# Kernel optimization log

Measured on AMD Instinct MI355X. Metric: run time of the kernel, lower is better.

## Reference

```python
import jax, jax.numpy as jnp
import numpy as np

B, S, IN, D, H, L, DFF, NT, K = 32, 512, 256, 512, 8, 2, 2048, 424, 25
DK = D // H


def moving_avg_trend(x, k):
    # AvgPool1d(kernel=k, stride=1, pad=k//2, count_include_pad=False) along seq axis
    b, s, d = x.shape
    half = k // 2
    cs = jnp.cumsum(x, axis=1)
    cs = jnp.concatenate([jnp.zeros((b, 1, d), x.dtype), cs], axis=1)  # [b, s+1, d]
    idx = jnp.arange(s)
    hi = jnp.minimum(idx + half + 1, s)
    lo = jnp.maximum(idx - half, 0)
    win = cs[:, hi] - cs[:, lo]                    # windowed sums [b, s, d]
    cnt = (hi - lo).astype(x.dtype)
    return win / cnt[None, :, None]


def auto_correlation(x, qkvo_w, qkvo_b):
    b, s, d = x.shape
    Q = (x @ qkvo_w[0] + qkvo_b[0]).reshape(b, s, H, DK)
    Kt = (x @ qkvo_w[1] + qkvo_b[1]).reshape(b, s, H, DK)
    V = (x @ qkvo_w[2] + qkvo_b[2]).reshape(b, s, H, DK)
    Qf = jnp.fft.rfft(Q, axis=1)
    Kf = jnp.fft.rfft(Kt, axis=1)
    corr = jnp.fft.irfft(Qf * jnp.conj(Kf), n=s, axis=1)
    corr = jax.nn.softmax(corr, axis=1)
    out = (corr * V).reshape(b, s, d)
    return out @ qkvo_w[3] + qkvo_b[3]


def encoder_layer(x, qkvo_w, qkvo_b, w1, b1, w2, b2):
    x_corr = auto_correlation(x, qkvo_w, qkvo_b)
    y = x + x_corr
    x = y - moving_avg_trend(y, K)                 # seasonal component (decomp1)
    ffn = jax.nn.gelu(x @ w1 + b1) @ w2 + b2
    y = x + ffn
    x = y - moving_avg_trend(y, K)                 # decomp2
    return x


def setup_inputs() -> dict:
    key = jax.random.key(0)
    ks = jax.random.split(key, 16)
    sc = 0.02
    return {
        "x": jax.random.normal(ks[0], (B, S, IN), jnp.float32),
        "embed_w": jax.random.normal(ks[1], (IN, D), jnp.float32) * sc,
        "embed_b": jnp.zeros((D,), jnp.float32),
        "qkvo_w": jax.random.normal(ks[2], (L, 4, D, D), jnp.float32) * sc,
        "qkvo_b": jnp.zeros((L, 4, D), jnp.float32),
        "ffn_w1": jax.random.normal(ks[3], (L, D, DFF), jnp.float32) * sc,
        "ffn_b1": jnp.zeros((L, DFF), jnp.float32),
        "ffn_w2": jax.random.normal(ks[4], (L, DFF, D), jnp.float32) * sc,
        "ffn_b2": jnp.zeros((L, D), jnp.float32),
        "proj_w1": jax.random.normal(ks[5], (D, D // 2), jnp.float32) * sc,
        "proj_b1": jnp.zeros((D // 2,), jnp.float32),
        "proj_w2": jax.random.normal(ks[6], (D // 2, NT), jnp.float32) * sc,
        "proj_b2": jnp.zeros((NT,), jnp.float32),
    }


def reference(x, embed_w, embed_b, qkvo_w, qkvo_b, ffn_w1, ffn_b1, ffn_w2, ffn_b2,
              proj_w1, proj_b1, proj_w2, proj_b2):
    h = x @ embed_w + embed_b
    for l in range(L):
        h = encoder_layer(h, qkvo_w[l], qkvo_b[l], ffn_w1[l], ffn_b1[l], ffn_w2[l], ffn_b2[l])
    h = h.mean(axis=1)                             # [B, D]
    h = jax.nn.relu(h @ proj_w1 + proj_b1)
    return h @ proj_w2 + proj_b2                   # [B, NT]
```

## Files before the change

### kernel.cpp

```cpp
#include <hip/hip_runtime.h>
#include <hip/hip_bf16.h>

#define S_LEN 512
#define D_DIM 512
#define B_DIM 32
#define IN_DIM 256
#define DFF_DIM 2048
#define NT_DIM 424

static constexpr size_t SZ = (size_t)B_DIM * S_LEN * D_DIM;

using s8v = __attribute__((ext_vector_type(8))) short;
using f4v = __attribute__((ext_vector_type(4))) float;
typedef unsigned short ushortT;

__device__ __forceinline__ ushortT f2bf(float f) {
  unsigned u = __float_as_uint(f);
  u += 0x7FFFu + ((u >> 16) & 1u);
  return (ushortT)(u >> 16);
}
__device__ __forceinline__ float bf2f(ushortT h) {
  return __uint_as_float(((unsigned)h) << 16);
}

__device__ __forceinline__ float gelu_fast(float x) {
  float a = 1.5957691216057308f * (x + 0.044715f * x * x * x);
  return x / (1.f + __expf(-a));
}

__device__ __forceinline__ float2 cadd(float2 a, float2 b) { return float2{a.x + b.x, a.y + b.y}; }
__device__ __forceinline__ float2 csub(float2 a, float2 b) { return float2{a.x - b.x, a.y - b.y}; }
__device__ __forceinline__ float2 cmul(float2 a, float2 b) {
  return float2{a.x * b.x - a.y * b.y, a.x * b.y + a.y * b.x};
}
__device__ __forceinline__ float2 mni(float2 a) { return float2{a.y, -a.x}; }

__device__ __forceinline__ void dft8(float2 a[8]) {
  float2 t0 = cadd(a[0], a[4]), t4 = csub(a[0], a[4]);
  float2 t1 = cadd(a[1], a[5]), t5 = csub(a[1], a[5]);
  float2 t2 = cadd(a[2], a[6]), t6 = csub(a[2], a[6]);
  float2 t3 = cadd(a[3], a[7]), t7 = csub(a[3], a[7]);
  float2 u0 = cadd(t0, t2), u2 = csub(t0, t2);
  float2 u1 = cadd(t1, t3), u3 = csub(t1, t3);
  const float C = 0.70710678118654752f;
  float2 s5 = float2{C * (t5.x + t5.y), C * (t5.y - t5.x)};
  float2 s6 = mni(t6);
  float2 s7 = float2{C * (t7.y - t7.x), -C * (t7.x + t7.y)};
  float2 v0 = cadd(t4, s6), v2 = csub(t4, s6);
  float2 v1 = cadd(s5, s7), v3 = csub(s5, s7);
  a[0] = cadd(u0, u1); a[4] = csub(u0, u1);
  a[2] = cadd(u2, mni(u3)); a[6] = csub(u2, mni(u3));
  a[1] = cadd(v0, v1); a[5] = csub(v0, v1);
  a[3] = cadd(v2, mni(v3)); a[7] = csub(v2, mni(v3));
}

__global__ __launch_bounds__(256) void conv_all(
    const float* __restrict__ embed_w, const float* __restrict__ qkvo_w,
    const float* __restrict__ ffn_w1, const float* __restrict__ ffn_w2,
    ushortT* __restrict__ embed_wt, ushortT* __restrict__ qkvo_wt,
    ushortT* __restrict__ ffn1_wt, ushortT* __restrict__ ffn2_wt)
{
  __shared__ float T[32][33];
  const int z = blockIdx.z;
  const float* W; ushortT* Wt; int Kp, N;
  if (z == 0)       { W = embed_w; Wt = embed_wt; Kp = 256; N = 512; }
  else if (z <= 8)  { int i = z - 1; W = qkvo_w + (size_t)i * 512 * 512;
                      Wt = qkvo_wt + (size_t)i * 512 * 512; Kp = 512; N = 512; }
  else if (z <= 10) { int l = z - 9; W = ffn_w1 + (size_t)l * 512 * 2048;
                      Wt = ffn1_wt + (size_t)l * 2048 * 512; Kp = 512; N = 2048; }
  else              { int l = z - 11; W = ffn_w2 + (size_t)l * 2048 * 512;
                      Wt = ffn2_wt + (size_t)l * 512 * 2048; Kp = 2048; N = 512; }
  int k0, n0;
  if (z >= 11) { k0 = blockIdx.y * 32; n0 = blockIdx.x * 32; }
  else         { k0 = blockIdx.x * 32; n0 = blockIdx.y * 32; }
  if (k0 >= Kp || n0 >= N) return;

  const int tid = threadIdx.x;
  const int col = tid & 31, r8 = tid >> 5;
#pragma unroll
  for (int it = 0; it < 4; ++it) {
    int row = r8 + it * 8;
    T[row][col] = W[(size_t)(k0 + row) * N + n0 + col];
  }
  __syncthreads();
  const int nl = tid >> 3, kq = tid & 7;
#pragma unroll
  for (int j = 0; j < 4; ++j) {
    int kl = kq * 4 + j;
    Wt[(size_t)(n0 + nl) * Kp + k0 + kl] = f2bf(T[kl][nl]);
  }
}

__global__ __launch_bounds__(256) void cvt_bf16(
    const float* __restrict__ in, ushortT* __restrict__ out, int n4)
{
  int i = blockIdx.x * 256 + threadIdx.x;
  if (i >= n4) return;
  float4 v = ((const float4*)in)[i];
  ushortT o[4] = {f2bf(v.x), f2bf(v.y), f2bf(v.z), f2bf(v.w)};
  *(uint2*)&out[(size_t)i * 4] = *(const uint2*)o;
}

template<int ACT, int RES, int OUT>
__global__ __launch_bounds__(256) void gemm_bf16(
    const ushortT* __restrict__ A, const ushortT* __restrict__ Wt,
    const float* __restrict__ bias, const float* __restrict__ res,
    const ushortT* __restrict__ resb,
    float* __restrict__ C, ushortT* __restrict__ Cb,
    ushortT* __restrict__ Qh, ushortT* __restrict__ Kh, int M, int Kp, int N)
{
  __shared__ __align__(16) ushortT smem[24576];
  ushortT* Tt = smem;

  const int tid = threadIdx.x;
  const int lane = tid & 63, wid = tid >> 6;
  const int fr = lane & 15, kq = lane >> 4;
  const int wr = wid >> 1, wc = wid & 1;

  const int nwg = gridDim.x * gridDim.y;
  const int bid = blockIdx.y * gridDim.x + blockIdx.x;
  const int swz = (bid & 7) * (nwg >> 3) + (bid >> 3);
  const int bx = swz % gridDim.x, by = swz / gridDim.x;
  const int m0 = by * 128, n0 = bx * 128;

  int srow[2], skq[2];
#pragma unroll
  for (int t = 0; t < 2; ++t) {
    int ch = wid * 2 + t;
    int row = ch * 16 + (lane >> 2);
    int kql = lane & 3;
    srow[t] = row;
    skq[t] = kql ^ ((row >> 1) & 3);
  }

  int aoff[4], boff[4];
#pragma unroll
  for (int i = 0; i < 4; ++i) {
    int ra = wr * 64 + i * 16 + fr;
    aoff[i] = ra * 32 + ((kq ^ ((ra >> 1) & 3)) << 3);
    int rb = wc * 64 + i * 16 + fr;
    boff[i] = rb * 32 + ((kq ^ ((rb >> 1) & 3)) << 3);
  }

  auto STAGE = [&](int buf, int k0) {
#pragma unroll
    for (int t = 0; t < 2; ++t) {
      const ushortT* as = A + (size_t)(m0 + srow[t]) * Kp + k0 + skq[t] * 8;
      __builtin_amdgcn_global_load_lds(
          (const __attribute__((address_space(1))) unsigned int*)as,
          (__attribute__((address_space(3))) unsigned int*)&smem[buf * 4096 + (wid * 2 + t) * 512],
          16, 0, 0);
      const ushortT* wsrc = Wt + (size_t)(n0 + srow[t]) * Kp + k0 + skq[t] * 8;
      __builtin_amdgcn_global_load_lds(
          (const __attribute__((address_space(1))) unsigned int*)wsrc,
          (__attribute__((address_space(3))) unsigned int*)&smem[12288 + buf * 4096 + (wid * 2 + t) * 512],
          16, 0, 0);
    }
  };

  f4v acc[4][4] = {};
  STAGE(0, 0);
  if (Kp > 32) STAGE(1, 32);
  int cur = 0, nxt = 2;

  for (int k0 = 0; k0 < Kp; k0 += 32) {
    if (k0 + 32 < Kp) {
      asm volatile("s_waitcnt vmcnt(4)" ::: "memory");
    } else {
      asm volatile("s_waitcnt vmcnt(0)" ::: "memory");
    }
    __builtin_amdgcn_s_barrier();
    __builtin_amdgcn_sched_barrier(0);
    if (k0 + 64 < Kp) {
      STAGE(nxt, k0 + 64);
      nxt = (nxt == 2) ? 0 : nxt + 1;
    }
    s8v af[4], bfv[4];
    const int ab = cur * 4096, wb = 12288 + cur * 4096;
#pragma unroll
    for (int i = 0; i < 4; ++i) {
      af[i]  = *(const s8v*)&smem[ab + aoff[i]];
      bfv[i] = *(const s8v*)&smem[wb + boff[i]];
    }
#pragma unroll
    for (int i = 0; i < 4; ++i)
#pragma unroll
      for (int j = 0; j < 4; ++j)
        acc[i][j] = __builtin_amdgcn_mfma_f32_16x16x32_bf16(af[i], bfv[j], acc[i][j], 0, 0, 0);
    cur = (cur == 2) ? 0 : cur + 1;
  }

  if (OUT == 3 && n0 < 1024) {
    __syncthreads();
#pragma unroll
    for (int j = 0; j < 4; ++j) {
      const int c = wc * 64 + j * 16 + fr;
      const float bv = bias[n0 + c];
#pragma unroll
      for (int i = 0; i < 4; ++i)
#pragma unroll
        for (int r = 0; r < 4; ++r) {
          const int s = wr * 64 + i * 16 + kq * 4 + r;
          _Float16 hh = (_Float16)(acc[i][j][r] + bv);
          Tt[c * 132 + s] = __builtin_bit_cast(ushortT, hh);
        }
    }
    __syncthreads();
    ushortT* dstM = (n0 < 512) ? Qh : Kh;
    const int cg0 = n0 & 511;
    const int bb = m0 >> 9, ss0 = m0 & 511;
    const int g = tid >> 4, ln = tid & 15;
#pragma unroll
    for (int p = 0; p < 8; ++p) {
      const int c = p * 16 + g;
      uint4 v = *(const uint4*)&Tt[c * 132 + ln * 8];
      *(uint4*)&dstM[((size_t)bb * 512 + cg0 + c) * 512 + ss0 + ln * 8] = v;
    }
  } else {
    constexpr bool WB16 = (OUT != 0);
    const int nb  = (OUT == 3) ? 512 : N;
    const int cb0 = (OUT == 3) ? (n0 - 1024) : n0;
    if (WB16) __syncthreads();
#pragma unroll
    for (int j = 0; j < 4; ++j) {
      const int lc = wc * 64 + j * 16 + fr;
      const int gc = n0 + lc;
      const float bv = bias[gc];
#pragma unroll
      for (int i = 0; i < 4; ++i)
#pragma unroll
        for (int r = 0; r < 4; ++r) {
          const int lr = wr * 64 + i * 16 + kq * 4 + r;
          const int gr = m0 + lr;
          float v = acc[i][j][r] + bv;
          if (RES == 1) v += res[(size_t)gr * N + gc];
          if (RES == 2) v += bf2f(resb[(size_t)gr * N + gc]);
          if (ACT == 1) v = gelu_fast(v);
          if (OUT == 0 || OUT == 1) C[(size_t)gr * N + gc] = v;
          if (WB16) Tt[lr * 132 + lc] = f2bf(v);
        }
    }
    if (WB16) {
      __syncthreads();
      const int g = tid >> 4, ln = tid & 15;
#pragma unroll
      for (int p = 0; p < 8; ++p) {
        const int row = p * 16 + g;
        uint4 v = *(const uint4*)&Tt[row * 132 + ln * 8];
        *(uint4*)&Cb[(size_t)(m0 + row) * nb + cb0 + ln * 8] = v;
      }
    }
  }
}

__global__ __launch_bounds__(512) void autocorr_fft(
    const ushortT* __restrict__ Qh, const ushortT* __restrict__ Kh,
    const ushortT* __restrict__ Vb, ushortT* __restrict__ Ob)
{
  __shared__ float2 zs[8 * 578];
  const int tid = threadIdx.x;
  const int b  = blockIdx.x >> 6;
  const int c0 = (blockIdx.x & 63) << 3;
  const int ch = tid >> 6;
  const int t  = tid & 63;
  float2* zc = &zs[ch * 578];

  {
    const ushortT* Qg = Qh + ((size_t)b * 512 + c0 + ch) * 512 + t * 8;
    const ushortT* Kg = Kh + ((size_t)b * 512 + c0 + ch) * 512 + t * 8;
    uint4 qv = *(const uint4*)Qg;
    uint4 kv = *(const uint4*)Kg;
    const ushortT* qp = (const ushortT*)&qv;
    const ushortT* kp = (const ushortT*)&kv;
    const int base = 9 * t;
#pragma unroll
    for (int j = 0; j < 8; ++j) {
      zc[base + j] = float2{(float)__builtin_bit_cast(_Float16, qp[j]),
                            (float)__builtin_bit_cast(_Float16, kp[j])};
    }
  }
  __syncthreads();

  float2 a[8];
  auto stage_fn = [&](int stage, bool do_scatter) {
#pragma unroll
    for (int r = 0; r < 8; ++r) { int ci = t + 64 * r; a[r] = zc[ci + (ci >> 3)]; }
    dft8(a);
    if (stage < 2) {
      float angle = (stage == 0) ? (-6.283185307179586f / 512.f) * (float)t
                                 : (-6.283185307179586f / 64.f) * (float)(t >> 3);
      float sn, cs;
      __sincosf(angle, &sn, &cs);
      float2 w = float2{cs, sn}, wp = w;
      a[1] = cmul(a[1], wp);
#pragma unroll
      for (int r = 2; r < 8; ++r) { wp = cmul(wp, w); a[r] = cmul(a[r], wp); }
    }
    if (!do_scatter) return;
    __syncthreads();
#pragma unroll
    for (int r = 0; r < 8; ++r) {
      int ci = (stage == 0) ? 8 * t + r
             : (stage == 1) ? (t & 7) + 64 * (t >> 3) + 8 * r
                            : t + 64 * r;
      zc[ci + (ci >> 3)] = a[r];
    }
    __syncthreads();
  };

  stage_fn(0, true); stage_fn(1, true); stage_fn(2, true);

  float2 Zk[8], Zm[8];
#pragma unroll
  for (int r = 0; r < 8; ++r) {
    int k = t + 64 * r, mk = (512 - k) & 511;
    Zk[r] = zc[k + (k >> 3)];
    Zm[r] = zc[mk + (mk >> 3)];
  }
  __syncthreads();
  const float S = 0.00048828125f;
#pragma unroll
  for (int r = 0; r < 8; ++r) {
    int k = t + 64 * r;
    float x1 = Zk[r].x, y1 = Zk[r].y, x2 = Zm[r].x, y2 = Zm[r].y;
    float sx = x1 + x2, dx = x1 - x2, sy = y1 + y2, dy = y1 - y2;
    float pre = sx * sy - dy * dx;
    float pim = sx * dx + dy * sy;
    zc[k + (k >> 3)] = float2{pre * S, -pim * S};
  }
  __syncthreads();

  stage_fn(0, true); stage_fn(1, true); stage_fn(2, false);

  float corr[8];
#pragma unroll
  for (int r = 0; r < 8; ++r) corr[r] = a[r].x;
  float mx = corr[0];
#pragma unroll
  for (int r = 1; r < 8; ++r) mx = fmaxf(mx, corr[r]);
#pragma unroll
  for (int o = 1; o < 64; o <<= 1) mx = fmaxf(mx, __shfl_xor(mx, o));
  float ex[8], sum = 0.f;
#pragma unroll
  for (int r = 0; r < 8; ++r) { ex[r] = __expf(corr[r] - mx); sum += ex[r]; }
#pragma unroll
  for (int o = 1; o < 64; o <<= 1) sum += __shfl_xor(sum, o);
  const float inv = 1.f / sum;

  __syncthreads();
  float* wl = (float*)zc;
#pragma unroll
  for (int r = 0; r < 8; ++r) wl[t + 64 * r] = ex[r] * inv;
  __syncthreads();

  const float* wall = (const float*)zs;
  const size_t base = (size_t)b * S_LEN * D_DIM + c0;
  for (int i = tid; i < 4096; i += 512) {
    int s = i >> 3, cc = i & 7;
    float wv = wall[cc * 1156 + s];
    size_t ad = base + (size_t)s * D_DIM + cc;
    Ob[ad] = f2bf(wv * bf2f(Vb[ad]));
  }
}

template<int MEAN, int WF>
__global__ __launch_bounds__(256) void movavg_sub2(
    const float* __restrict__ y, float* __restrict__ outf,
    ushortT* __restrict__ outb, float* __restrict__ hm)
{
  __shared__ float ys[512 * 32];
  const int tid = threadIdx.x;
  const int b = blockIdx.y, d0 = blockIdx.x * 32;
  const float* yb = y + (size_t)b * S_LEN * D_DIM + d0;

#pragma unroll 4
  for (int p = 0; p < 16; ++p) {
    int i = p * 256 + tid;
    int s = i >> 3, dq = i & 7;
    float4 v = *(const float4*)(yb + (size_t)s * D_DIM + dq * 4);
    *(float4*)&ys[s * 32 + dq * 4] = v;
  }
  __syncthreads();

  const int d = tid & 31, sg = tid >> 5;
  const int s0 = sg * 64;
  int lo = max(s0 - 12, 0), hi = min(s0 + 13, S_LEN);
  float sum = 0.f;
  for (int t = lo; t < hi; ++t) sum += ys[t * 32 + d];

  float msum = 0.f;
  const size_t gb = (size_t)b * S_LEN * D_DIM + d0 + d;
  for (int i = 0; i < 64; ++i) {
    const int s = s0 + i;
    float val = ys[s * 32 + d] - sum / (float)(hi - lo);
    size_t g = gb + (size_t)s * D_DIM;
    if (WF) outf[g] = val;
    outb[g] = f2bf(val);
    if (MEAN) msum += val;
    int add = s + 13;
    if (add < S_LEN) { sum += ys[add * 32 + d]; hi = add + 1; }
    int rem = s - 12;
    if (rem >= 0) { sum -= ys[rem * 32 + d]; lo = rem + 1; }
  }
  if (MEAN) atomicAdd(&hm[b * D_DIM + d0 + d], msum * (1.f / (float)S_LEN));
}

__global__ __launch_bounds__(256) void proj_head1(
    const float* __restrict__ hm, const float* __restrict__ W1,
    const float* __restrict__ b1, float* __restrict__ p1)
{
  __shared__ float hs[32 * 512];
  const int tid = threadIdx.x, n0 = blockIdx.x * 32;
  for (int i = tid; i < 16384; i += 256) hs[i] = hm[i];
  __syncthreads();
  const int n = tid & 31, mg = tid >> 5;
  float acc[4] = {};
  for (int k = 0; k < 512; ++k) {
    float w = W1[(size_t)k * 256 + n0 + n];
#pragma unroll
    for (int mi = 0; mi < 4; ++mi)
      acc[mi] = fmaf(hs[(mg * 4 + mi) * 512 + k], w, acc[mi]);
  }
  const float bb = b1[n0 + n];
#pragma unroll
  for (int mi = 0; mi < 4; ++mi)
    p1[(size_t)(mg * 4 + mi) * 256 + n0 + n] = fmaxf(acc[mi] + bb, 0.f);
}

__global__ __launch_bounds__(256) void proj_head2(
    const float* __restrict__ p1, const float* __restrict__ W2,
    const float* __restrict__ b2, float* __restrict__ out)
{
  __shared__ float ps[32 * 256];
  const int tid = threadIdx.x;
  for (int i = tid; i < 8192; i += 256) ps[i] = p1[i];
  __syncthreads();
  const int n = tid & 31, mg = tid >> 5;
  const int ng = blockIdx.x * 32 + n;
  const bool ok = ng < NT_DIM;
  float acc[4] = {};
  for (int k = 0; k < 256; ++k) {
    float w = ok ? W2[(size_t)k * NT_DIM + ng] : 0.f;
#pragma unroll
    for (int mi = 0; mi < 4; ++mi)
      acc[mi] = fmaf(ps[(mg * 4 + mi) * 256 + k], w, acc[mi]);
  }
  if (ok) {
    const float bb = b2[ng];
#pragma unroll
    for (int mi = 0; mi < 4; ++mi)
      out[(size_t)(mg * 4 + mi) * NT_DIM + ng] = acc[mi] + bb;
  }
}

extern "C" void kernel_launch(void* const* d_in, const int* in_sizes, int n_in,
                              void* d_out, int out_size, void* d_ws, size_t ws_size,
                              hipStream_t stream)
{
  const float* x       = (const float*)d_in[0];
  const float* embed_w = (const float*)d_in[1];
  const float* embed_b = (const float*)d_in[2];
  const float* qkvo_w  = (const float*)d_in[3];
  const float* qkvo_b  = (const float*)d_in[4];
  const float* ffn_w1  = (const float*)d_in[5];
  const float* ffn_b1  = (const float*)d_in[6];
  const float* ffn_w2  = (const float*)d_in[7];
  const float* ffn_b2  = (const float*)d_in[8];
  const float* proj_w1 = (const float*)d_in[9];
  const float* proj_b1 = (const float*)d_in[10];
  const float* proj_w2 = (const float*)d_in[11];
  const float* proj_b2 = (const float*)d_in[12];
  float* out = (float*)d_out;

  float* ws = (float*)d_ws;
  float* Bv = ws;
  float* Bh = ws + SZ;
  float* Bq = ws + 2 * SZ;
  float* Bk = ws + 3 * SZ;
  ushortT* Sb = (ushortT*)(ws + 4 * SZ);
  ushortT* Wb = (ushortT*)(ws + 4 * SZ + SZ / 2);
  ushortT* embed_wt = Wb;
  ushortT* qkvo_wt  = embed_wt + (size_t)512 * 256;
  ushortT* ffn1_wt  = qkvo_wt + (size_t)8 * 512 * 512;
  ushortT* ffn2_wt  = ffn1_wt + (size_t)2 * 2048 * 512;
  float* hm = (float*)(ffn2_wt + (size_t)2 * 512 * 2048);
  float* p1 = hm + 16384;
  ushortT* Hb  = (ushortT*)Bv;
  ushortT* Vb  = (ushortT*)Bv;
  ushortT* xb  = (ushortT*)Bq;
  ushortT* QKh = (ushortT*)Bq;

  dim3 blk(256);

  hipMemsetAsync(hm, 0, 16384 * sizeof(float), stream);

  conv_all<<<dim3(16, 64, 13), blk, 0, stream>>>(
      embed_w, qkvo_w, ffn_w1, ffn_w2, embed_wt, qkvo_wt, ffn1_wt, ffn2_wt);

  cvt_bf16<<<dim3(4096), blk, 0, stream>>>(x, xb, B_DIM * S_LEN * IN_DIM / 4);

  gemm_bf16<0, 0, 1><<<dim3(4, 128), blk, 0, stream>>>(
      xb, embed_wt, embed_b, nullptr, nullptr, Bh, Sb, nullptr, nullptr,
      16384, IN_DIM, D_DIM);

  for (int l = 0; l < 2; ++l) {
    const ushortT* qw = qkvo_wt + (size_t)l * 4 * 512 * 512;
    const float* qb = qkvo_b + (size_t)l * 4 * 512;
    gemm_bf16<0, 0, 3><<<dim3(12, 128), blk, 0, stream>>>(
        Sb, qw, qb, nullptr, nullptr, nullptr, Vb, QKh, QKh + SZ,
        16384, 512, 1536);
    autocorr_fft<<<dim3(B_DIM * 64), dim3(512), 0, stream>>>(QKh, QKh + SZ, Vb, Sb);
    gemm_bf16<0, 1, 0><<<dim3(4, 128), blk, 0, stream>>>(
        Sb, qw + (size_t)3 * 512 * 512, qb + 1536, Bh, nullptr, Bq, nullptr,
        nullptr, nullptr, 16384, 512, 512);
    movavg_sub2<0, 0><<<dim3(16, 32), blk, 0, stream>>>(Bq, nullptr, Sb, nullptr);
    gemm_bf16<1, 0, 2><<<dim3(16, 128), blk, 0, stream>>>(
        Sb, ffn1_wt + (size_t)l * 2048 * 512, ffn_b1 + (size_t)l * DFF_DIM,
        nullptr, nullptr, nullptr, Hb, nullptr, nullptr, 16384, 512, 2048);
    gemm_bf16<0, 2, 0><<<dim3(4, 128), blk, 0, stream>>>(
        Hb, ffn2_wt + (size_t)l * 512 * 2048, ffn_b2 + (size_t)l * D_DIM,
        nullptr, Sb, Bq, nullptr, nullptr, nullptr, 16384, 2048, 512);
    if (l == 1)
      movavg_sub2<1, 1><<<dim3(16, 32), blk, 0, stream>>>(Bq, Bh, Sb, hm);
    else
      movavg_sub2<0, 1><<<dim3(16, 32), blk, 0, stream>>>(Bq, Bh, Sb, nullptr);
  }

  proj_head1<<<dim3(8), blk, 0, stream>>>(hm, proj_w1, proj_b1, p1);
  proj_head2<<<dim3(14), blk, 0, stream>>>(p1, proj_w2, proj_b2, out);
}
```

Before: 553.3 us.

## Add 256x256-tile pipelined FFN1 GEMM with direct global-to-LDS loads

Replaces the generic 128-tile bf16 GEMM for the first FFN projection with a dedicated kernel. It uses 256x256 output tiles, 512 threads, double-buffered LDS filled through global_load_lds, and four phases per K step with explicit vmcnt waits and barriers. It also adds an XOR-swizzled LDS layout, a block-id swizzle for L2 locality, and a fused bias+GELU epilogue staged through LDS. The aim is more operand reuse per tile and overlap of loads with MFMA work. The cost is 128 KB of dynamic LDS and heavy register use, which limits occupancy and relies on hand-tuned wait counts.

```diff
diff --git a/kernel.cpp b/kernel.cpp
--- a/kernel.cpp
+++ b/kernel.cpp
@@ -253,6 +253,142 @@
   }
 }
 
+__global__ __launch_bounds__(512, 2) void gemm_ffn1_256(
+    const ushortT* __restrict__ A, const ushortT* __restrict__ Wt,
+    const float* __restrict__ bias, ushortT* __restrict__ Cb,
+    int M, int Kp, int N)
+{
+  extern __shared__ ushortT smem[];
+  const int tid = threadIdx.x;
+  const int lane = tid & 63, wid = tid >> 6;
+  const int fr = lane & 15, kq = lane >> 4;
+  const int wm = wid >> 2, wn = wid & 3;
+
+  const int nwg = gridDim.x * gridDim.y;
+  const int bid = blockIdx.y * gridDim.x + blockIdx.x;
+  const int swz = (bid & 7) * (nwg >> 3) + (bid >> 3);
+  const int bx = swz % gridDim.x, by = swz / gridDim.x;
+  const int m0 = by * 256, n0 = bx * 256;
+
+  const int KT = Kp >> 6;
+
+  const int srow = wid * 8 + (lane >> 3);
+  const int sch = (lane & 7) ^ ((lane >> 3) & 7);
+
+  auto STAGE_A = [&](int b, int u, int kt) {
+    const ushortT* src = A + (size_t)(m0 + u * 64 + srow) * Kp + kt * 64 + sch * 8;
+    __builtin_amdgcn_global_load_lds(
+        (const __attribute__((address_space(1))) unsigned int*)src,
+        (__attribute__((address_space(3))) unsigned int*)
+            &smem[((b * 2 + (u >> 1)) * 128 + (u & 1) * 64) * 64 + wid * 512],
+        16, 0, 0);
+  };
+  auto STAGE_B = [&](int b, int u, int kt) {
+    const ushortT* src = Wt + (size_t)(n0 + u * 64 + srow) * Kp + kt * 64 + sch * 8;
+    __builtin_amdgcn_global_load_lds(
+        (const __attribute__((address_space(1))) unsigned int*)src,
+        (__attribute__((address_space(3))) unsigned int*)
+            &smem[32768 + ((b * 2 + (u >> 1)) * 128 + (u & 1) * 64) * 64 + wid * 512],
+        16, 0, 0);
+  };
+
+  f4v acc[8][4] = {};
+  s8v bcar[2][2];
+
+  STAGE_A(0, 0, 0); STAGE_A(0, 2, 0);
+  STAGE_B(0, 0, 0); STAGE_B(0, 1, 0);
+  STAGE_A(0, 1, 0); STAGE_A(0, 3, 0);
+  STAGE_B(0, 2, 0); STAGE_B(0, 3, 0);
+
+  auto phase = [&](int ph, int b, bool st, int kt) {
+    if (st) {
+      if (ph == 0)      { STAGE_A(b ^ 1, 0, kt + 1); STAGE_A(b ^ 1, 2, kt + 1); }
+      else if (ph == 1) { STAGE_B(b ^ 1, 0, kt + 1); STAGE_B(b ^ 1, 1, kt + 1); }
+      else if (ph == 2) { STAGE_A(b ^ 1, 1, kt + 1); STAGE_A(b ^ 1, 3, kt + 1); }
+      else              { STAGE_B(b ^ 1, 2, kt + 1); STAGE_B(b ^ 1, 3, kt + 1); }
+    }
+    if (st) {
+      asm volatile("s_waitcnt vmcnt(6)" ::: "memory");
+    } else {
+      if (ph == 0)      asm volatile("s_waitcnt vmcnt(4)" ::: "memory");
+      else if (ph == 1) asm volatile("s_waitcnt vmcnt(2)" ::: "memory");
+      else if (ph == 2) asm volatile("s_waitcnt vmcnt(0)" ::: "memory");
+    }
+    __builtin_amdgcn_s_barrier();
+    asm volatile("" ::: "memory");
+
+    const int i0 = (ph & 1) * 4;
+    const int jp = ph >> 1;
+    if ((ph & 1) == 0) {
+#pragma unroll
+      for (int jj = 0; jj < 2; ++jj) {
+        int col = jp * 128 + wn * 32 + jj * 16 + fr;
+        int rbase = 32768 + ((b * 2 + (col >> 7)) * 128 + (col & 127)) * 64;
+#pragma unroll
+        for (int ks = 0; ks < 2; ++ks)
+          bcar[jj][ks] = *(const s8v*)&smem[rbase + (((ks * 4 + kq) ^ (fr & 7)) << 3)];
+      }
+    }
+    s8v av[4][2];
+    const int ab = (b * 2 + wm) * 8192;
+#pragma unroll
+    for (int ii = 0; ii < 4; ++ii) {
+      int rl = (i0 + ii) * 16 + fr;
+#pragma unroll
+      for (int ks = 0; ks < 2; ++ks)
+        av[ii][ks] = *(const s8v*)&smem[ab + rl * 64 + (((ks * 4 + kq) ^ (fr & 7)) << 3)];
+    }
+    __builtin_amdgcn_s_setprio(1);
+#pragma unroll
+    for (int ii = 0; ii < 4; ++ii)
+#pragma unroll
+      for (int jj = 0; jj < 2; ++jj)
+#pragma unroll
+        for (int ks = 0; ks < 2; ++ks)
+          acc[i0 + ii][jp * 2 + jj] = __builtin_amdgcn_mfma_f32_16x16x32_bf16(
+              av[ii][ks], bcar[jj][ks], acc[i0 + ii][jp * 2 + jj], 0, 0, 0);
+    __builtin_amdgcn_s_setprio(0);
+  };
+
+  for (int kt = 0; kt < KT; ++kt) {
+    const int b = kt & 1;
+    const bool st = (kt + 1 < KT);
+    phase(0, b, st, kt);
+    phase(1, b, st, kt);
+    phase(2, b, st, kt);
+    phase(3, b, st, kt);
+  }
+
+  ushortT* Tt = smem;
+#pragma unroll
+  for (int p = 0; p < 2; ++p) {
+    __syncthreads();
+    if (wm == p) {
+#pragma unroll
+      for (int j = 0; j < 4; ++j) {
+        const int col = (j < 2) ? (wn * 32 + j * 16 + fr)
+                                : (128 + wn * 32 + (j - 2) * 16 + fr);
+        const float bv = bias[n0 + col];
+#pragma unroll
+        for (int i = 0; i < 8; ++i)
+#pragma unroll
+          for (int r = 0; r < 4; ++r) {
+            const int rl = i * 16 + kq * 4 + r;
+            Tt[rl * 264 + col] = f2bf(gelu_fast(acc[i][j][r] + bv));
+          }
+      }
+    }
+    __syncthreads();
+#pragma unroll
+    for (int q = 0; q < 8; ++q) {
+      int idx = q * 512 + tid;
+      int row = idx >> 5, c = idx & 31;
+      uint4 v = *(const uint4*)&Tt[row * 264 + c * 8];
+      *(uint4*)&Cb[(size_t)(m0 + p * 128 + row) * N + n0 + c * 8] = v;
+    }
+  }
+}
+
 __global__ __launch_bounds__(512) void autocorr_fft(
     const ushortT* __restrict__ Qh, const ushortT* __restrict__ Kh,
     const ushortT* __restrict__ Vb, ushortT* __restrict__ Ob)
@@ -492,6 +628,9 @@
 
   dim3 blk(256);
 
+  hipFuncSetAttribute((const void*)gemm_ffn1_256,
+                      hipFuncAttributeMaxDynamicSharedMemorySize, 131072);
+
   hipMemsetAsync(hm, 0, 16384 * sizeof(float), stream);
 
   conv_all<<<dim3(16, 64, 13), blk, 0, stream>>>(
@@ -514,9 +653,9 @@
         Sb, qw + (size_t)3 * 512 * 512, qb + 1536, Bh, nullptr, Bq, nullptr,
         nullptr, nullptr, 16384, 512, 512);
     movavg_sub2<0, 0><<<dim3(16, 32), blk, 0, stream>>>(Bq, nullptr, Sb, nullptr);
-    gemm_bf16<1, 0, 2><<<dim3(16, 128), blk, 0, stream>>>(
+    gemm_ffn1_256<<<dim3(8, 64), dim3(512), 131072, stream>>>(
         Sb, ffn1_wt + (size_t)l * 2048 * 512, ffn_b1 + (size_t)l * DFF_DIM,
-        nullptr, nullptr, nullptr, Hb, nullptr, nullptr, 16384, 512, 2048);
+        Hb, 16384, 512, 2048);
     gemm_bf16<0, 2, 0><<<dim3(4, 128), blk, 0, stream>>>(
         Hb, ffn2_wt + (size_t)l * 512 * 2048, ffn_b2 + (size_t)l * D_DIM,
         nullptr, Sb, Bq, nullptr, nullptr, nullptr, 16384, 2048, 512);
```

Measured after the change: 570.0 us. 3.0% more time.

## Keep residual stream in bf16 and drop fp32 activation buffers

Applied to the files above, without the earlier changes.

The residual/hidden stream now lives only in bf16. GEMMs write bf16 outputs with bf16 residual adds instead of fp32 C buffers, and the moving-average kernel reads bf16 and writes a single bf16 output. Shared memory is padded to a stride of 33. This roughly halves global traffic for the residual, out-projection and FFN2 outputs and the movavg passes, but it adds bf16 rounding to the residual path, which may reduce accuracy.

```diff
diff --git a/kernel.cpp b/kernel.cpp
--- a/kernel.cpp
+++ b/kernel.cpp
@@ -104,8 +104,7 @@
 template<int ACT, int RES, int OUT>
 __global__ __launch_bounds__(256) void gemm_bf16(
     const ushortT* __restrict__ A, const ushortT* __restrict__ Wt,
-    const float* __restrict__ bias, const float* __restrict__ res,
-    const ushortT* __restrict__ resb,
+    const float* __restrict__ bias, const ushortT* __restrict__ resb,
     float* __restrict__ C, ushortT* __restrict__ Cb,
     ushortT* __restrict__ Qh, ushortT* __restrict__ Kh, int M, int Kp, int N)
 {
@@ -233,10 +232,9 @@
           const int lr = wr * 64 + i * 16 + kq * 4 + r;
           const int gr = m0 + lr;
           float v = acc[i][j][r] + bv;
-          if (RES == 1) v += res[(size_t)gr * N + gc];
           if (RES == 2) v += bf2f(resb[(size_t)gr * N + gc]);
           if (ACT == 1) v = gelu_fast(v);
-          if (OUT == 0 || OUT == 1) C[(size_t)gr * N + gc] = v;
+          if (OUT == 1) C[(size_t)gr * N + gc] = v;
           if (WB16) Tt[lr * 132 + lc] = f2bf(v);
         }
     }
@@ -363,22 +361,24 @@
   }
 }
 
-template<int MEAN, int WF>
-__global__ __launch_bounds__(256) void movavg_sub2(
-    const float* __restrict__ y, float* __restrict__ outf,
-    ushortT* __restrict__ outb, float* __restrict__ hm)
-{
-  __shared__ float ys[512 * 32];
+template<int MEAN>
+__global__ __launch_bounds__(256) void movavg_bf16(
+    const ushortT* __restrict__ y, ushortT* __restrict__ outb,
+    float* __restrict__ hm)
+{
+  __shared__ float ys[512 * 33];
   const int tid = threadIdx.x;
   const int b = blockIdx.y, d0 = blockIdx.x * 32;
-  const float* yb = y + (size_t)b * S_LEN * D_DIM + d0;
-
-#pragma unroll 4
-  for (int p = 0; p < 16; ++p) {
+  const ushortT* yb = y + (size_t)b * S_LEN * D_DIM + d0;
+
+#pragma unroll
+  for (int p = 0; p < 8; ++p) {
     int i = p * 256 + tid;
-    int s = i >> 3, dq = i & 7;
-    float4 v = *(const float4*)(yb + (size_t)s * D_DIM + dq * 4);
-    *(float4*)&ys[s * 32 + dq * 4] = v;
+    int s = i >> 2, dq = i & 3;
+    uint4 v = *(const uint4*)(yb + (size_t)s * D_DIM + dq * 8);
+    const ushortT* hp = (const ushortT*)&v;
+#pragma unroll
+    for (int j = 0; j < 8; ++j) ys[s * 33 + dq * 8 + j] = bf2f(hp[j]);
   }
   __syncthreads();
 
@@ -386,21 +386,19 @@
   const int s0 = sg * 64;
   int lo = max(s0 - 12, 0), hi = min(s0 + 13, S_LEN);
   float sum = 0.f;
-  for (int t = lo; t < hi; ++t) sum += ys[t * 32 + d];
+  for (int t = lo; t < hi; ++t) sum += ys[t * 33 + d];
 
   float msum = 0.f;
   const size_t gb = (size_t)b * S_LEN * D_DIM + d0 + d;
   for (int i = 0; i < 64; ++i) {
     const int s = s0 + i;
-    float val = ys[s * 32 + d] - sum / (float)(hi - lo);
-    size_t g = gb + (size_t)s * D_DIM;
-    if (WF) outf[g] = val;
-    outb[g] = f2bf(val);
+    float val = ys[s * 33 + d] - sum / (float)(hi - lo);
+    outb[gb + (size_t)s * D_DIM] = f2bf(val);
     if (MEAN) msum += val;
     int add = s + 13;
-    if (add < S_LEN) { sum += ys[add * 32 + d]; hi = add + 1; }
+    if (add < S_LEN) { sum += ys[add * 33 + d]; hi = add + 1; }
     int rem = s - 12;
-    if (rem >= 0) { sum -= ys[rem * 32 + d]; lo = rem + 1; }
+    if (rem >= 0) { sum -= ys[rem * 33 + d]; lo = rem + 1; }
   }
   if (MEAN) atomicAdd(&hm[b * D_DIM + d0 + d], msum * (1.f / (float)S_LEN));
 }
@@ -474,7 +472,6 @@
 
   float* ws = (float*)d_ws;
   float* Bv = ws;
-  float* Bh = ws + SZ;
   float* Bq = ws + 2 * SZ;
   float* Bk = ws + 3 * SZ;
   ushortT* Sb = (ushortT*)(ws + 4 * SZ);
@@ -489,6 +486,8 @@
   ushortT* Vb  = (ushortT*)Bv;
   ushortT* xb  = (ushortT*)Bq;
   ushortT* QKh = (ushortT*)Bq;
+  ushortT* Yb  = (ushortT*)Bq;
+  ushortT* Xb  = (ushortT*)Bk;
 
   dim3 blk(256);
 
@@ -499,31 +498,30 @@
 
   cvt_bf16<<<dim3(4096), blk, 0, stream>>>(x, xb, B_DIM * S_LEN * IN_DIM / 4);
 
-  gemm_bf16<0, 0, 1><<<dim3(4, 128), blk, 0, stream>>>(
-      xb, embed_wt, embed_b, nullptr, nullptr, Bh, Sb, nullptr, nullptr,
+  gemm_bf16<0, 0, 2><<<dim3(4, 128), blk, 0, stream>>>(
+      xb, embed_wt, embed_b, nullptr, nullptr, Xb, nullptr, nullptr,
       16384, IN_DIM, D_DIM);
 
   for (int l = 0; l < 2; ++l) {
     const ushortT* qw = qkvo_wt + (size_t)l * 4 * 512 * 512;
     const float* qb = qkvo_b + (size_t)l * 4 * 512;
     gemm_bf16<0, 0, 3><<<dim3(12, 128), blk, 0, stream>>>(
-        Sb, qw, qb, nullptr, nullptr, nullptr, Vb, QKh, QKh + SZ,
-        16384, 512, 1536);
+        Xb, qw, qb, nullptr, nullptr, Vb, QKh, QKh + SZ, 16384, 512, 1536);
     autocorr_fft<<<dim3(B_DIM * 64), dim3(512), 0, stream>>>(QKh, QKh + SZ, Vb, Sb);
-    gemm_bf16<0, 1, 0><<<dim3(4, 128), blk, 0, stream>>>(
-        Sb, qw + (size_t)3 * 512 * 512, qb + 1536, Bh, nullptr, Bq, nullptr,
+    gemm_bf16<0, 2, 2><<<dim3(4, 128), blk, 0, stream>>>(
+        Sb, qw + (size_t)3 * 512 * 512, qb + 1536, Xb, nullptr, Yb,
         nullptr, nullptr, 16384, 512, 512);
-    movavg_sub2<0, 0><<<dim3(16, 32), blk, 0, stream>>>(Bq, nullptr, Sb, nullptr);
+    movavg_bf16<0><<<dim3(16, 32), blk, 0, stream>>>(Yb, Sb, nullptr);
     gemm_bf16<1, 0, 2><<<dim3(16, 128), blk, 0, stream>>>(
         Sb, ffn1_wt + (size_t)l * 2048 * 512, ffn_b1 + (size_t)l * DFF_DIM,
-        nullptr, nullptr, nullptr, Hb, nullptr, nullptr, 16384, 512, 2048);
-    gemm_bf16<0, 2, 0><<<dim3(4, 128), blk, 0, stream>>>(
+        nullptr, nullptr, Hb, nullptr, nullptr, 16384, 512, 2048);
+    gemm_bf16<0, 2, 2><<<dim3(4, 128), blk, 0, stream>>>(
         Hb, ffn2_wt + (size_t)l * 512 * 2048, ffn_b2 + (size_t)l * D_DIM,
-        nullptr, Sb, Bq, nullptr, nullptr, nullptr, 16384, 2048, 512);
+        Sb, nullptr, Yb, nullptr, nullptr, 16384, 2048, 512);
     if (l == 1)
-      movavg_sub2<1, 1><<<dim3(16, 32), blk, 0, stream>>>(Bq, Bh, Sb, hm);
+      movavg_bf16<1><<<dim3(16, 32), blk, 0, stream>>>(Yb, Xb, hm);
     else
-      movavg_sub2<0, 1><<<dim3(16, 32), blk, 0, stream>>>(Bq, Bh, Sb, nullptr);
+      movavg_bf16<0><<<dim3(16, 32), blk, 0, stream>>>(Yb, Xb, nullptr);
   }
 
   proj_head1<<<dim3(8), blk, 0, stream>>>(hm, proj_w1, proj_b1, p1);
```

Result: no change. 544.7 us (-1.6%).
